# Kernel tuning notes

Hardware: AMD Instinct MI355X
Metric: run time of the kernel (lower is better)

The kernel has to match this reference:

```python
import jax, jax.numpy as jnp
import numpy as np

N = 8192
H = 1024
E = 8
K = 2

def setup_inputs() -> dict:
    key = jax.random.key(0)
    ks = jax.random.split(key, 8)
    x = jax.random.normal(ks[0], (N, H), dtype=jnp.float32)
    grad = jax.random.normal(ks[1], (N, 1), dtype=jnp.float32)
    s_r = 1.0 / np.sqrt(H + 1)
    s1 = 1.0 / np.sqrt(H)
    s2 = 1.0 / np.sqrt(4 * H)
    Wr = jax.random.normal(ks[2], (H + 1, E), dtype=jnp.float32) * s_r
    br = jnp.zeros((E,), dtype=jnp.float32)
    W1 = jax.random.normal(ks[3], (E, H, 4 * H), dtype=jnp.float32) * s1
    b1 = jnp.zeros((E, 4 * H), dtype=jnp.float32)
    W2 = jax.random.normal(ks[4], (E, 4 * H, H), dtype=jnp.float32) * s2
    b2 = jnp.zeros((E, H), dtype=jnp.float32)
    return {"x": x, "grad": grad, "Wr": Wr, "br": br, "W1": W1, "b1": b1, "W2": W2, "b2": b2}

def reference(x, grad, Wr, br, W1, b1, W2, b2):
    # router on [x, grad]
    router_in = jnp.concatenate([x, grad], axis=-1)            # [N, H+1]
    logits = router_in @ Wr + br                               # [N, E]
    probs = jax.nn.softmax(logits, axis=-1)
    topk_probs, topk_idx = jax.lax.top_k(probs, K)             # [N, K]
    # combine weight per (token, expert): sum over k of prob * onehot(idx)
    onehot = jax.nn.one_hot(topk_idx, E, dtype=x.dtype)        # [N, K, E]
    cw = jnp.einsum('nk,nke->ne', topk_probs, onehot)          # [N, E]
    # dense all-expert MLP (equivalent math to masked dispatch/scatter-add)
    h = jnp.einsum('nh,ehf->enf', x, W1) + b1[:, None, :]      # [E, N, 4H]
    h = jax.nn.gelu(h, approximate=False)                      # torch nn.GELU = exact erf
    o = jnp.einsum('enf,efh->enh', h, W2) + b2[:, None, :]     # [E, N, H]
    out = jnp.einsum('enh,ne->nh', o, cw)                      # [N, H]
    return out
```

## Files before the change

### kernel.cpp

```cpp
#include <hip/hip_runtime.h>
#include <hip/hip_bf16.h>
#include <stdint.h>


#define NTOK 8192
#define HD   1024
#define NE   8
#define FF   4096
#define MAXT 72

typedef float  f32x4 __attribute__((ext_vector_type(4)));
typedef _Float16 half8 __attribute__((ext_vector_type(8)));
typedef _Float16 half4 __attribute__((ext_vector_type(4)));

#define AS1 __attribute__((address_space(1)))
#define AS3 __attribute__((address_space(3)))

__device__ __forceinline__ void gload16(const void* g, void* l) {
  __builtin_amdgcn_global_load_lds((AS1 void*)g, (AS3 void*)l, 16, 0, 0);
}

__device__ __forceinline__ bool tile_lookup(const int* __restrict__ counts,
                                            int t, int& e, int& m0, int& cnt) {
#pragma unroll
  for (int i = 0; i < NE; ++i) {
    int c = counts[i];
    int nt = (c + 255) >> 8;
    if (t < nt) { e = i; m0 = t << 8; cnt = c; return true; }
    t -= nt;
  }
  return false;
}

__global__ __launch_bounds__(256) void transc_k(const float* __restrict__ src,
                                                _Float16* __restrict__ dst,
                                                int R, int C) {
  __shared__ float t[64][65];
  const int e = blockIdx.z;
  const size_t eb = (size_t)e * R * C;
  const int r0 = blockIdx.y * 64, c0 = blockIdx.x * 64;
  const int tid = threadIdx.x;
#pragma unroll
  for (int i = 0; i < 4; ++i) {
    int idx = tid + i * 256;
    int r = idx >> 4, c = (idx & 15) * 4;
    float4 v = *(const float4*)(src + eb + (size_t)(r0 + r) * C + (c0 + c));
    t[r][c] = v.x; t[r][c + 1] = v.y; t[r][c + 2] = v.z; t[r][c + 3] = v.w;
  }
  __syncthreads();
#pragma unroll
  for (int i = 0; i < 4; ++i) {
    int idx = tid + i * 256;
    int cr = idx >> 4, r4 = (idx & 15) * 4;
    half4 o = {(_Float16)t[r4][cr], (_Float16)t[r4 + 1][cr],
               (_Float16)t[r4 + 2][cr], (_Float16)t[r4 + 3][cr]};
    *(half4*)(dst + eb + (size_t)(c0 + cr) * R + (r0 + r4)) = o;
  }
}

__global__ __launch_bounds__(256) void router_k(const float* __restrict__ x,
                                                const float* __restrict__ grad,
                                                const float* __restrict__ Wr,
                                                const float* __restrict__ br,
                                                int* __restrict__ counts,
                                                int* __restrict__ tokL,
                                                float* __restrict__ wL,
                                                _Float16* __restrict__ xh) {
  const int lane = threadIdx.x & 63;
  const int n = blockIdx.x * 4 + (threadIdx.x >> 6);
  float acc[8] = {0.f, 0.f, 0.f, 0.f, 0.f, 0.f, 0.f, 0.f};
  const float* xr = x + (size_t)n * HD;
  _Float16* xo = xh + (size_t)n * HD;
#pragma unroll 4
  for (int i = 0; i < 16; ++i) {
    float xv = xr[i * 64 + lane];
    xo[i * 64 + lane] = (_Float16)xv;
    const float* wr = Wr + (size_t)(i * 64 + lane) * NE;
    float4 w0 = *(const float4*)wr;
    float4 w1 = *(const float4*)(wr + 4);
    acc[0] += xv * w0.x; acc[1] += xv * w0.y; acc[2] += xv * w0.z; acc[3] += xv * w0.w;
    acc[4] += xv * w1.x; acc[5] += xv * w1.y; acc[6] += xv * w1.z; acc[7] += xv * w1.w;
  }
#pragma unroll
  for (int off = 32; off > 0; off >>= 1)
#pragma unroll
    for (int e = 0; e < 8; ++e) acc[e] += __shfl_xor(acc[e], off, 64);
  if (lane == 0) {
    float gv = grad[n];
    float lg[8];
#pragma unroll
    for (int e = 0; e < 8; ++e) lg[e] = acc[e] + gv * Wr[HD * NE + e] + br[e];
    float m = lg[0];
#pragma unroll
    for (int e = 1; e < 8; ++e) m = fmaxf(m, lg[e]);
    float s = 0.f, p[8];
#pragma unroll
    for (int e = 0; e < 8; ++e) { p[e] = expf(lg[e] - m); s += p[e]; }
    int i1 = 0;
#pragma unroll
    for (int e = 1; e < 8; ++e) if (lg[e] > lg[i1]) i1 = e;
    int i2 = (i1 == 0) ? 1 : 0;
#pragma unroll
    for (int e = 0; e < 8; ++e) if (e != i1 && lg[e] > lg[i2]) i2 = e;
    float inv = 1.0f / s;
    int p1 = atomicAdd(&counts[i1], 1);
    tokL[i1 * NTOK + p1] = n; wL[i1 * NTOK + p1] = p[i1] * inv;
    int p2 = atomicAdd(&counts[i2], 1);
    tokL[i2 * NTOK + p2] = n; wL[i2 * NTOK + p2] = p[i2] * inv;
  }
}

__global__ void prefix_k(const int* __restrict__ counts, int* __restrict__ base) {
  if (threadIdx.x == 0) {
    int s = 0;
    for (int e = 0; e < NE; ++e) { base[e] = s; s += counts[e]; }
  }
}


#define DSA(BUF, MH)                                                          \
  {                                                                           \
    const char* _ab = smem + (BUF)*65536 + (MH)*16384;                        \
    _Pragma("unroll") for (int mf = 0; mf < 4; ++mf) {                        \
      int row = wm * 64 + mf * 16 + lr;                                       \
      _Pragma("unroll") for (int k2 = 0; k2 < 2; ++k2) {                      \
        int off = row * 128 + ((k2 * 64 + (lk << 4)) ^ ((row & 7) << 4));     \
        af[mf][k2] = *(const half8*)(_ab + off);                              \
      }                                                                       \
    }                                                                         \
  }

#define DSB(BUF, NH, BF)                                                      \
  {                                                                           \
    const char* _bb = smem + (BUF)*65536 + 32768 + (NH)*16384;                \
    _Pragma("unroll") for (int nf = 0; nf < 2; ++nf) {                        \
      int row = wn * 32 + nf * 16 + lr;                                       \
      _Pragma("unroll") for (int k2 = 0; k2 < 2; ++k2) {                      \
        int off = row * 128 + ((k2 * 64 + (lk << 4)) ^ ((row & 7) << 4));     \
        BF[nf][k2] = *(const half8*)(_bb + off);                              \
      }                                                                       \
    }                                                                         \
  }

#define MFMAQ(MH, NH, BF)                                                     \
  __builtin_amdgcn_s_setprio(1);                                              \
  _Pragma("unroll") for (int mf = 0; mf < 4; ++mf)                            \
  _Pragma("unroll") for (int nf = 0; nf < 2; ++nf)                            \
  _Pragma("unroll") for (int k2 = 0; k2 < 2; ++k2)                            \
    acc[(MH)*4 + mf][(NH)*2 + nf] = __builtin_amdgcn_mfma_f32_16x16x32_f16(   \
        af[mf][k2], BF[nf][k2], acc[(MH)*4 + mf][(NH)*2 + nf], 0, 0, 0);      \
  __builtin_amdgcn_s_setprio(0);

#define PH(DS, MH, NH, BF, STG, VM)                                           \
  do {                                                                        \
    DS;                                                                       \
    STG;                                                                      \
    if (VM) asm volatile("s_waitcnt vmcnt(4)" ::: "memory");                  \
    __builtin_amdgcn_s_barrier();                                             \
    asm volatile("s_waitcnt lgkmcnt(0)" ::: "memory");                        \
    MFMAQ(MH, NH, BF);                                                        \
    __builtin_amdgcn_s_barrier();                                             \
  } while (0)

#define STAGE_A(BUF, H, KIDX)                                                 \
  {                                                                           \
    char* _d = smem + (BUF)*65536 + (H)*16384 + (wid << 10);                  \
    gload16(aP[(H)*2 + 0] + (KIDX)*64, _d);                                   \
    gload16(aP[(H)*2 + 1] + (KIDX)*64, _d + 8192);                            \
  }
#define STAGE_B(BUF, H, KIDX, LDB)                                            \
  {                                                                           \
    char* _d = smem + (BUF)*65536 + 32768 + (H)*16384 + (wid << 10);          \
    gload16(bP + (size_t)((H)*128) * (LDB) + (KIDX)*64, _d);                  \
    gload16(bP + (size_t)((H)*128 + 64) * (LDB) + (KIDX)*64, _d + 8192);      \
  }

#define ITER8(T1, T0N, T1N, LDB)                                              \
  PH(DSA(0, 0); DSB(0, 0, bf0), 0, 0, bf0, STAGE_A(1, 1, T1), 0);             \
  PH(DSB(0, 1, bf1),            0, 1, bf1, STAGE_B(1, 0, T1, LDB), 0);        \
  PH(DSA(0, 1),                 1, 1, bf1, STAGE_A(0, 0, T0N), 0);            \
  PH(,                          1, 0, bf0, STAGE_B(0, 1, T0N, LDB), 1);       \
  PH(DSA(1, 0); DSB(1, 0, bf0), 0, 0, bf0, STAGE_A(0, 1, T0N), 0);            \
  PH(DSB(1, 1, bf1),            0, 1, bf1, STAGE_B(0, 0, T0N, LDB), 0);       \
  PH(DSA(1, 1),                 1, 1, bf1, STAGE_A(1, 0, T1N), 0);            \
  PH(,                          1, 0, bf0, STAGE_B(1, 1, T1N, LDB), 1);

__global__ __launch_bounds__(512, 2) void gemm1_k(const _Float16* __restrict__ xh,
                                                  const _Float16* __restrict__ w1t,
                                                  const float* __restrict__ b1,
                                                  const int* __restrict__ tokL,
                                                  const int* __restrict__ counts,
                                                  const int* __restrict__ base,
                                                  _Float16* __restrict__ hbuf) {
  int e, m0, cnt;
  if (!tile_lookup(counts, blockIdx.y, e, m0, cnt)) return;
  const int n0 = blockIdx.x * 256;
  const int hb = base[e];

  __shared__ __align__(16) char smem[131072];

  const int tid = threadIdx.x;
  const int lane = tid & 63;
  const int wid = tid >> 6;
  const int wm = wid & 1, wn = wid >> 1;
  const int lr = lane & 15, lk = lane >> 4;

  const int srow = tid >> 3;
  const int kk = ((tid & 7) ^ (srow & 7)) << 3;
  const _Float16* aP[4];
#pragma unroll
  for (int h = 0; h < 2; ++h)
#pragma unroll
    for (int j = 0; j < 2; ++j) {
      int r = h * 128 + j * 64 + srow;
      int gm = m0 + r; if (gm >= cnt) gm = cnt - 1;
      aP[h * 2 + j] = xh + (size_t)tokL[e * NTOK + gm] * HD + kk;
    }
  const _Float16* bP = w1t + ((size_t)e * FF + n0 + srow) * HD + kk;

  f32x4 acc[8][4] = {};
  half8 af[4][2], bf0[2][2], bf1[2][2];

  STAGE_A(0, 0, 0); STAGE_A(0, 1, 0); STAGE_B(0, 0, 0, HD); STAGE_B(0, 1, 0, HD);
  STAGE_A(1, 0, 1); STAGE_B(1, 1, 1, HD);
  asm volatile("s_waitcnt vmcnt(4)" ::: "memory");
  __builtin_amdgcn_s_barrier();

  const int NK = HD / 64;
  for (int it = 0; it < NK / 2; ++it) {
    int t1 = 2 * it + 1;
    int t0n = 2 * it + 2; if (t0n > NK - 1) t0n = NK - 1;
    int t1n = 2 * it + 3; if (t1n > NK - 1) t1n = NK - 1;
    ITER8(t1, t0n, t1n, HD);
  }
  asm volatile("s_waitcnt vmcnt(0) lgkmcnt(0)" ::: "memory");
  __builtin_amdgcn_s_barrier();

#pragma unroll
  for (int ni = 0; ni < 4; ++ni) {
    const int nh = ni >> 1, nf = ni & 1;
    int col = nh * 128 + wn * 32 + nf * 16 + lr;
    float bias = b1[(size_t)e * FF + n0 + col];
#pragma unroll
    for (int mi = 0; mi < 8; ++mi) {
      const int mh = mi >> 2, mf = mi & 3;
      int rb = mh * 128 + wm * 64 + mf * 16 + lk * 4;
#pragma unroll
      for (int j = 0; j < 4; ++j) {
        float v = acc[mi][ni][j] + bias;
        v = 0.5f * v * (1.0f + erff(v * 0.70710678118654752f));
        int row = rb + j;
        *(_Float16*)(smem + row * 512 + ((col * 2) ^ ((row & 7) << 4))) = (_Float16)v;
      }
    }
  }
  asm volatile("s_waitcnt lgkmcnt(0)" ::: "memory");
  __builtin_amdgcn_s_barrier();
#pragma unroll
  for (int ps = 0; ps < 16; ++ps) {
    int row = ps * 16 + (tid >> 5);
    int c = tid & 31;
    int lc = c ^ (row & 7);
    half8 v = *(const half8*)(smem + row * 512 + c * 16);
    int gm = m0 + row;
    if (gm < cnt)
      *(half8*)(hbuf + (size_t)(hb + gm) * FF + n0 + lc * 8) = v;
  }
}

__global__ __launch_bounds__(512, 2) void gemm2_k(const _Float16* __restrict__ hbuf,
                                                  const _Float16* __restrict__ w2t,
                                                  const float* __restrict__ b2,
                                                  const int* __restrict__ tokL,
                                                  const float* __restrict__ wL,
                                                  const int* __restrict__ counts,
                                                  const int* __restrict__ base,
                                                  float* __restrict__ out) {
  int e, m0, cnt;
  if (!tile_lookup(counts, blockIdx.y, e, m0, cnt)) return;
  const int n0 = blockIdx.x * 256;
  const int ks = blockIdx.z;
  const int hb = base[e];

  __shared__ __align__(16) char smem[131072];

  const int tid = threadIdx.x;
  const int lane = tid & 63;
  const int wid = tid >> 6;
  const int wm = wid & 1, wn = wid >> 1;
  const int lr = lane & 15, lk = lane >> 4;

  const int srow = tid >> 3;
  const int kk = ((tid & 7) ^ (srow & 7)) << 3;
  const size_t kbase = (size_t)ks * 2048;
  const _Float16* aP[4];
#pragma unroll
  for (int h = 0; h < 2; ++h)
#pragma unroll
    for (int j = 0; j < 2; ++j) {
      int r = h * 128 + j * 64 + srow;
      int gm = m0 + r; if (gm >= cnt) gm = cnt - 1;
      aP[h * 2 + j] = hbuf + (size_t)(hb + gm) * FF + kbase + kk;
    }
  const _Float16* bP = w2t + ((size_t)e * HD + n0 + srow) * FF + kbase + kk;

  f32x4 acc[8][4] = {};
  half8 af[4][2], bf0[2][2], bf1[2][2];

  STAGE_A(0, 0, 0); STAGE_A(0, 1, 0); STAGE_B(0, 0, 0, FF); STAGE_B(0, 1, 0, FF);
  STAGE_A(1, 0, 1); STAGE_B(1, 1, 1, FF);
  asm volatile("s_waitcnt vmcnt(4)" ::: "memory");
  __builtin_amdgcn_s_barrier();

  const int NK = 2048 / 64;
  for (int it = 0; it < NK / 2; ++it) {
    int t1 = 2 * it + 1;
    int t0n = 2 * it + 2; if (t0n > NK - 1) t0n = NK - 1;
    int t1n = 2 * it + 3; if (t1n > NK - 1) t1n = NK - 1;
    ITER8(t1, t0n, t1n, FF);
  }
  asm volatile("s_waitcnt vmcnt(0) lgkmcnt(0)" ::: "memory");
  __builtin_amdgcn_s_barrier();

  float b2v[4];
#pragma unroll
  for (int ni = 0; ni < 4; ++ni) {
    const int nh = ni >> 1, nf = ni & 1;
    int n = n0 + nh * 128 + wn * 32 + nf * 16 + lr;
    b2v[ni] = (ks == 0) ? b2[(size_t)e * HD + n] : 0.0f;
  }
#pragma unroll
  for (int mi = 0; mi < 8; ++mi) {
    const int mh = mi >> 2, mf = mi & 3;
    int rb = m0 + mh * 128 + wm * 64 + mf * 16 + lk * 4;
    int tk[4]; float pw[4]; bool ok[4];
#pragma unroll
    for (int j = 0; j < 4; ++j) {
      int gm = rb + j;
      ok[j] = (gm < cnt);
      int idx = e * NTOK + (ok[j] ? gm : 0);
      tk[j] = tokL[idx];
      pw[j] = wL[idx];
    }
#pragma unroll
    for (int ni = 0; ni < 4; ++ni) {
      const int nh = ni >> 1, nf = ni & 1;
      int n = n0 + nh * 128 + wn * 32 + nf * 16 + lr;
#pragma unroll
      for (int j = 0; j < 4; ++j) {
        if (ok[j])
          atomicAdd(out + (size_t)tk[j] * HD + n, pw[j] * (acc[mi][ni][j] + b2v[ni]));
      }
    }
  }
}

extern "C" void kernel_launch(void* const* d_in, const int* in_sizes, int n_in,
                              void* d_out, int out_size, void* d_ws, size_t ws_size,
                              hipStream_t stream) {
  const float* x    = (const float*)d_in[0];
  const float* grad = (const float*)d_in[1];
  const float* Wr   = (const float*)d_in[2];
  const float* br   = (const float*)d_in[3];
  const float* W1   = (const float*)d_in[4];
  const float* b1   = (const float*)d_in[5];
  const float* W2   = (const float*)d_in[6];
  const float* b2   = (const float*)d_in[7];
  float* out = (float*)d_out;

  char* ws = (char*)d_ws;
  int*      counts = (int*)(ws + 0);
  int*      basep  = (int*)(ws + 128);
  int*      tokL   = (int*)(ws + 256);
  float*    wL     = (float*)(ws + 262400);
  _Float16* xh     = (_Float16*)(ws + 524544);
  _Float16* w1t    = (_Float16*)(ws + 17301760);
  _Float16* w2t    = (_Float16*)(ws + 84410624);
  _Float16* hbuf   = (_Float16*)(ws + 151519488);
  if (ws_size < 285737216ull) return;

  hipMemsetAsync(counts, 0, 64, stream);
  hipMemsetAsync(out, 0, (size_t)NTOK * HD * 4, stream);

  transc_k<<<dim3(FF / 64, HD / 64, NE), 256, 0, stream>>>(W1, w1t, HD, FF);
  transc_k<<<dim3(HD / 64, FF / 64, NE), 256, 0, stream>>>(W2, w2t, FF, HD);
  router_k<<<NTOK / 4, 256, 0, stream>>>(x, grad, Wr, br, counts, tokL, wL, xh);
  prefix_k<<<1, 64, 0, stream>>>(counts, basep);

  gemm1_k<<<dim3(FF / 256, MAXT), 512, 0, stream>>>(xh, w1t, b1, tokL, counts, basep, hbuf);
  gemm2_k<<<dim3(HD / 256, MAXT, 2), 512, 0, stream>>>(hbuf, w2t, b2, tokL, wL, counts, basep, out);
}
```

Before: 1.022 ms.

## Replace atomic scatter-add MoE combine with fp16 staging and per-token gather

```diff
diff --git a/kernel.cpp b/kernel.cpp
--- a/kernel.cpp
+++ b/kernel.cpp
@@ -8,6 +8,7 @@
 #define NE   8
 #define FF   4096
 #define MAXT 72
+#define OBHALF ((size_t)NTOK * 2 * HD)
 
 typedef float  f32x4 __attribute__((ext_vector_type(4)));
 typedef _Float16 half8 __attribute__((ext_vector_type(8)));
@@ -62,9 +63,8 @@
                                                 const float* __restrict__ grad,
                                                 const float* __restrict__ Wr,
                                                 const float* __restrict__ br,
-                                                int* __restrict__ counts,
-                                                int* __restrict__ tokL,
-                                                float* __restrict__ wL,
+                                                int2* __restrict__ te,
+                                                float2* __restrict__ tp,
                                                 _Float16* __restrict__ xh) {
   const int lane = threadIdx.x & 63;
   const int n = blockIdx.x * 4 + (threadIdx.x >> 6);
@@ -103,11 +103,31 @@
 #pragma unroll
     for (int e = 0; e < 8; ++e) if (e != i1 && lg[e] > lg[i2]) i2 = e;
     float inv = 1.0f / s;
-    int p1 = atomicAdd(&counts[i1], 1);
-    tokL[i1 * NTOK + p1] = n; wL[i1 * NTOK + p1] = p[i1] * inv;
-    int p2 = atomicAdd(&counts[i2], 1);
-    tokL[i2 * NTOK + p2] = n; wL[i2 * NTOK + p2] = p[i2] * inv;
-  }
+    te[n] = make_int2(i1, i2);
+    tp[n] = make_float2(p[i1] * inv, p[i2] * inv);
+  }
+}
+
+__global__ __launch_bounds__(256) void build_k(const int2* __restrict__ te,
+                                               int* __restrict__ counts,
+                                               int* __restrict__ tokL,
+                                               int2* __restrict__ rowPos) {
+  __shared__ int hist[NE], cursor[NE], gbase[NE];
+  const int t = threadIdx.x;
+  if (t < NE) { hist[t] = 0; cursor[t] = 0; }
+  __syncthreads();
+  const int n = blockIdx.x * 256 + t;
+  int2 e = te[n];
+  atomicAdd(&hist[e.x], 1);
+  atomicAdd(&hist[e.y], 1);
+  __syncthreads();
+  if (t < NE) gbase[t] = atomicAdd(&counts[t], hist[t]);
+  __syncthreads();
+  int p1 = gbase[e.x] + atomicAdd(&cursor[e.x], 1);
+  tokL[e.x * NTOK + p1] = n;
+  int p2 = gbase[e.y] + atomicAdd(&cursor[e.y], 1);
+  tokL[e.y * NTOK + p2] = n;
+  rowPos[n] = make_int2(p1, p2);
 }
 
 __global__ void prefix_k(const int* __restrict__ counts, int* __restrict__ base) {
@@ -116,7 +136,6 @@
     for (int e = 0; e < NE; ++e) { base[e] = s; s += counts[e]; }
   }
 }
-
 
 #define DSA(BUF, MH)                                                          \
   {                                                                           \
@@ -192,9 +211,11 @@
                                                   const int* __restrict__ counts,
                                                   const int* __restrict__ base,
                                                   _Float16* __restrict__ hbuf) {
+  const int flat = blockIdx.x + (blockIdx.y << 4);
+  const int wg = (flat & 7) * 144 + (flat >> 3);
   int e, m0, cnt;
-  if (!tile_lookup(counts, blockIdx.y, e, m0, cnt)) return;
-  const int n0 = blockIdx.x * 256;
+  if (!tile_lookup(counts, wg >> 4, e, m0, cnt)) return;
+  const int n0 = (wg & 15) * 256;
   const int hb = base[e];
 
   __shared__ __align__(16) char smem[131072];
@@ -270,15 +291,14 @@
 
 __global__ __launch_bounds__(512, 2) void gemm2_k(const _Float16* __restrict__ hbuf,
                                                   const _Float16* __restrict__ w2t,
-                                                  const float* __restrict__ b2,
-                                                  const int* __restrict__ tokL,
-                                                  const float* __restrict__ wL,
                                                   const int* __restrict__ counts,
                                                   const int* __restrict__ base,
-                                                  float* __restrict__ out) {
+                                                  _Float16* __restrict__ obuf) {
+  const int flat = blockIdx.x + (blockIdx.y << 2);
+  const int wg = (flat & 7) * 36 + (flat >> 3);
   int e, m0, cnt;
-  if (!tile_lookup(counts, blockIdx.y, e, m0, cnt)) return;
-  const int n0 = blockIdx.x * 256;
+  if (!tile_lookup(counts, wg >> 2, e, m0, cnt)) return;
+  const int n0 = (wg & 3) * 256;
   const int ks = blockIdx.z;
   const int hb = base[e];
 
@@ -322,36 +342,73 @@
   asm volatile("s_waitcnt vmcnt(0) lgkmcnt(0)" ::: "memory");
   __builtin_amdgcn_s_barrier();
 
-  float b2v[4];
+  _Float16* ob = obuf + (size_t)ks * OBHALF;
 #pragma unroll
   for (int ni = 0; ni < 4; ++ni) {
     const int nh = ni >> 1, nf = ni & 1;
-    int n = n0 + nh * 128 + wn * 32 + nf * 16 + lr;
-    b2v[ni] = (ks == 0) ? b2[(size_t)e * HD + n] : 0.0f;
-  }
-#pragma unroll
-  for (int mi = 0; mi < 8; ++mi) {
-    const int mh = mi >> 2, mf = mi & 3;
-    int rb = m0 + mh * 128 + wm * 64 + mf * 16 + lk * 4;
-    int tk[4]; float pw[4]; bool ok[4];
-#pragma unroll
-    for (int j = 0; j < 4; ++j) {
-      int gm = rb + j;
-      ok[j] = (gm < cnt);
-      int idx = e * NTOK + (ok[j] ? gm : 0);
-      tk[j] = tokL[idx];
-      pw[j] = wL[idx];
-    }
-#pragma unroll
-    for (int ni = 0; ni < 4; ++ni) {
-      const int nh = ni >> 1, nf = ni & 1;
-      int n = n0 + nh * 128 + wn * 32 + nf * 16 + lr;
+    int col = nh * 128 + wn * 32 + nf * 16 + lr;
+#pragma unroll
+    for (int mi = 0; mi < 8; ++mi) {
+      const int mh = mi >> 2, mf = mi & 3;
+      int rb = mh * 128 + wm * 64 + mf * 16 + lk * 4;
 #pragma unroll
       for (int j = 0; j < 4; ++j) {
-        if (ok[j])
-          atomicAdd(out + (size_t)tk[j] * HD + n, pw[j] * (acc[mi][ni][j] + b2v[ni]));
+        int row = rb + j;
+        *(_Float16*)(smem + row * 512 + ((col * 2) ^ ((row & 7) << 4))) =
+            (_Float16)acc[mi][ni][j];
       }
     }
+  }
+  asm volatile("s_waitcnt lgkmcnt(0)" ::: "memory");
+  __builtin_amdgcn_s_barrier();
+#pragma unroll
+  for (int ps = 0; ps < 16; ++ps) {
+    int row = ps * 16 + (tid >> 5);
+    int c = tid & 31;
+    int lc = c ^ (row & 7);
+    half8 v = *(const half8*)(smem + row * 512 + c * 16);
+    int gm = m0 + row;
+    if (gm < cnt)
+      *(half8*)(ob + (size_t)(hb + gm) * HD + n0 + lc * 8) = v;
+  }
+}
+
+__global__ __launch_bounds__(512) void gather_k(const int2* __restrict__ te,
+                                                const float2* __restrict__ tp,
+                                                const int2* __restrict__ rowPos,
+                                                const int* __restrict__ base,
+                                                const float* __restrict__ b2,
+                                                const _Float16* __restrict__ obuf,
+                                                float* __restrict__ out) {
+  const int lane = threadIdx.x & 63;
+  const int n = blockIdx.x * 8 + (threadIdx.x >> 6);
+  const int2 e = te[n];
+  const float2 p = tp[n];
+  const int2 rp = rowPos[n];
+  const size_t r1 = (size_t)(base[e.x] + rp.x) * HD;
+  const size_t r2 = (size_t)(base[e.y] + rp.y) * HD;
+  const int c = lane * 16;
+  const _Float16* a1 = obuf + r1 + c;
+  const _Float16* a2 = obuf + r2 + c;
+  const float* b2a = b2 + (size_t)e.x * HD + c;
+  const float* b2b = b2 + (size_t)e.y * HD + c;
+  float* o = out + (size_t)n * HD + c;
+#pragma unroll
+  for (int q = 0; q < 2; ++q) {
+    half8 x10 = *(const half8*)(a1 + q * 8);
+    half8 x11 = *(const half8*)(a1 + OBHALF + q * 8);
+    half8 x20 = *(const half8*)(a2 + q * 8);
+    half8 x21 = *(const half8*)(a2 + OBHALF + q * 8);
+    float4 r0, r1v;
+#pragma unroll
+    for (int j = 0; j < 4; ++j) {
+      ((float*)&r0)[j] = p.x * ((float)x10[j] + (float)x11[j] + b2a[q * 8 + j]) +
+                         p.y * ((float)x20[j] + (float)x21[j] + b2b[q * 8 + j]);
+      ((float*)&r1v)[j] = p.x * ((float)x10[j + 4] + (float)x11[j + 4] + b2a[q * 8 + j + 4]) +
+                          p.y * ((float)x20[j + 4] + (float)x21[j + 4] + b2b[q * 8 + j + 4]);
+    }
+    *(float4*)(o + q * 8) = r0;
+    *(float4*)(o + q * 8 + 4) = r1v;
   }
 }
 
@@ -372,21 +429,25 @@
   int*      counts = (int*)(ws + 0);
   int*      basep  = (int*)(ws + 128);
   int*      tokL   = (int*)(ws + 256);
-  float*    wL     = (float*)(ws + 262400);
+  int2*     te     = (int2*)(ws + 262400);
+  float2*   tp     = (float2*)(ws + 327936);
+  int2*     rowPos = (int2*)(ws + 393472);
   _Float16* xh     = (_Float16*)(ws + 524544);
   _Float16* w1t    = (_Float16*)(ws + 17301760);
   _Float16* w2t    = (_Float16*)(ws + 84410624);
   _Float16* hbuf   = (_Float16*)(ws + 151519488);
+  _Float16* obuf   = (_Float16*)(ws + 17301760);
   if (ws_size < 285737216ull) return;
 
   hipMemsetAsync(counts, 0, 64, stream);
-  hipMemsetAsync(out, 0, (size_t)NTOK * HD * 4, stream);
 
   transc_k<<<dim3(FF / 64, HD / 64, NE), 256, 0, stream>>>(W1, w1t, HD, FF);
   transc_k<<<dim3(HD / 64, FF / 64, NE), 256, 0, stream>>>(W2, w2t, FF, HD);
-  router_k<<<NTOK / 4, 256, 0, stream>>>(x, grad, Wr, br, counts, tokL, wL, xh);
+  router_k<<<NTOK / 4, 256, 0, stream>>>(x, grad, Wr, br, te, tp, xh);
+  build_k<<<NTOK / 256, 256, 0, stream>>>(te, counts, tokL, rowPos);
   prefix_k<<<1, 64, 0, stream>>>(counts, basep);
 
   gemm1_k<<<dim3(FF / 256, MAXT), 512, 0, stream>>>(xh, w1t, b1, tokL, counts, basep, hbuf);
-  gemm2_k<<<dim3(HD / 256, MAXT, 2), 512, 0, stream>>>(hbuf, w2t, b2, tokL, wL, counts, basep, out);
-}
+  gemm2_k<<<dim3(HD / 256, MAXT, 2), 512, 0, stream>>>(hbuf, w2t, counts, basep, obuf);
+  gather_k<<<NTOK / 8, 512, 0, stream>>>(te, tp, rowPos, basep, b2, obuf, out);
+}
```

Measured after the change: 860.6 us. 15.8% less time.
